# Kernel tuning notes

Hardware: AMD Instinct MI355X
Metric: run time of the kernel (lower is better)

## Reference

```python
import jax, jax.numpy as jnp
import numpy as np

N_STATE = 1024
N_HEAD = 16
HEAD_DIM = N_STATE // N_HEAD


def setup_inputs() -> dict:
    key = jax.random.key(0)
    ks = jax.random.split(key, 8)
    s = 0.02
    return {
        "x": jax.random.normal(ks[0], (4, 1500, N_STATE), dtype=jnp.float32),
        "Wq": jax.random.normal(ks[1], (N_STATE, N_STATE), dtype=jnp.float32) * s,
        "bq": jnp.zeros((N_STATE,), dtype=jnp.float32),
        "Wk": jax.random.normal(ks[2], (N_STATE, N_STATE), dtype=jnp.float32) * s,
        "Wv": jax.random.normal(ks[3], (N_STATE, N_STATE), dtype=jnp.float32) * s,
        "bv": jnp.zeros((N_STATE,), dtype=jnp.float32),
        "Wo": jax.random.normal(ks[4], (N_STATE, N_STATE), dtype=jnp.float32) * s,
        "bo": jnp.zeros((N_STATE,), dtype=jnp.float32),
    }


def reference(x, Wq, bq, Wk, Wv, bv, Wo, bo):
    B, S, _ = x.shape
    scale = HEAD_DIM ** (-0.5)
    # projections (torch Linear: y = x @ W.T + b)
    q = x @ Wq.T + bq
    k = x @ Wk.T
    v = x @ Wv.T + bv
    # [B, H, S, D]
    q = q.reshape(B, S, N_HEAD, HEAD_DIM).transpose(0, 2, 1, 3)
    k = k.reshape(B, S, N_HEAD, HEAD_DIM).transpose(0, 2, 1, 3)
    v = v.reshape(B, S, N_HEAD, HEAD_DIM).transpose(0, 2, 1, 3)
    # scores scaled AFTER the matmul, as in the original (qk * qk_scale)
    qk = jnp.einsum("bhqd,bhkd->bhqk", q, k) * scale
    w = jax.nn.softmax(qk, axis=-1)
    wv = jnp.einsum("bhqk,bhkd->bhqd", w, v)
    wv = wv.transpose(0, 2, 1, 3).reshape(B, S, N_STATE)
    return wv @ Wo.T + bo
```

## Files before the change

### kernel.cpp

```cpp
#include <hip/hip_runtime.h>
#include <stdint.h>

#define S_LEN  1500
#define S_PAD  1536
#define BATCH  4
#define NSTATE 1024
#define NHEAD  16
#define HDIM   64
#define MROWS  6000
#define C1 0.180336879f

typedef __attribute__((ext_vector_type(8)))  short short8;
typedef __attribute__((ext_vector_type(4)))  float floatx4;
typedef __attribute__((ext_vector_type(16))) float floatx16;

__device__ __forceinline__ unsigned short f2bf(float f) {
  union { float f; unsigned int u; } v; v.f = f;
  unsigned int r = v.u + 0x7fffu + ((v.u >> 16) & 1u);
  return (unsigned short)(r >> 16);
}

__device__ __forceinline__ void gld_lds16(const void* g, void* l) {
  __builtin_amdgcn_global_load_lds(
      (const __attribute__((address_space(1))) void*)g,
      (__attribute__((address_space(3))) void*)l, 16, 0, 0);
}

__global__ __launch_bounds__(256) void cvt_all(
    const float* __restrict__ x,  const float* __restrict__ Wq,
    const float* __restrict__ Wk, const float* __restrict__ Wv,
    const float* __restrict__ Wo, unsigned short* __restrict__ dst)
{
  const size_t NX = (size_t)MROWS * NSTATE;
  size_t e = ((size_t)blockIdx.x * 256 + threadIdx.x) * 4;
  const float* src; size_t off;
  if (e < NX) { src = x; off = e; }
  else {
    size_t t = e - NX;
    int wsel = (int)(t >> 20);
    off = t & ((1u << 20) - 1);
    src = (wsel == 0) ? Wq : (wsel == 1) ? Wk : (wsel == 2) ? Wv : Wo;
  }
  float4 v = *(const float4*)(src + off);
  uint2 o;
  o.x = (unsigned int)f2bf(v.x) | ((unsigned int)f2bf(v.y) << 16);
  o.y = (unsigned int)f2bf(v.z) | ((unsigned int)f2bf(v.w) << 16);
  *(uint2*)(dst + e) = o;
}

template <bool F32OUT>
__device__ __forceinline__ void gemm128_bt(
    const unsigned short* __restrict__ X,
    const unsigned short* __restrict__ W,
    const float* __restrict__ bias,
    void* __restrict__ Yv,
    int m0, int n0, float oscale)
{
  __shared__ unsigned short As[2][128 * 32];
  __shared__ unsigned short Bs[2][128 * 32];

  const int tid  = threadIdx.x;
  const int lane = tid & 63;
  const int wid  = tid >> 6;
  const int wm   = (wid & 1) * 64;
  const int wn   = (wid >> 1) * 64;
  const int l15  = lane & 15;
  const int l4   = lane >> 4;

  floatx4 acc[4][4];
#pragma unroll
  for (int i = 0; i < 4; ++i)
#pragma unroll
    for (int j = 0; j < 4; ++j)
      acc[i][j] = (floatx4){0.f, 0.f, 0.f, 0.f};

  const int srow  = tid >> 2;
  const int scolb = (tid & 3) * 16;

  const char* xrp[2];
  const char* wrp[2];
#pragma unroll
  for (int r = 0; r < 2; ++r) {
    int arow = m0 + r * 64 + srow;
    if (arow > MROWS - 1) arow = MROWS - 1;
    xrp[r] = (const char*)X + (size_t)arow * NSTATE * 2 + scolb;
    int brow = n0 + r * 64 + srow;
    wrp[r] = (const char*)W + (size_t)brow * NSTATE * 2 + scolb;
  }

  for (int k0 = 0; k0 < NSTATE; k0 += 64) {
    __syncthreads();
#pragma unroll
    for (int h = 0; h < 2; ++h) {
      int kb = (k0 + h * 32) * 2;
#pragma unroll
      for (int r = 0; r < 2; ++r) {
        gld_lds16(xrp[r] + kb, (char*)As[h] + r * 4096 + wid * 1024);
        gld_lds16(wrp[r] + kb, (char*)Bs[h] + r * 4096 + wid * 1024);
      }
    }
    __syncthreads();

#pragma unroll
    for (int h = 0; h < 2; ++h) {
      short8 a[4], b[4];
#pragma unroll
      for (int i = 0; i < 4; ++i)
        a[i] = *(const short8*)(As[h] + (wm + i * 16 + l15) * 32 + l4 * 8);
#pragma unroll
      for (int j = 0; j < 4; ++j)
        b[j] = *(const short8*)(Bs[h] + (wn + j * 16 + l15) * 32 + l4 * 8);
#pragma unroll
      for (int i = 0; i < 4; ++i)
#pragma unroll
        for (int j = 0; j < 4; ++j)
          acc[i][j] = __builtin_amdgcn_mfma_f32_16x16x32_bf16(a[i], b[j], acc[i][j], 0, 0, 0);
    }
  }

#pragma unroll
  for (int j = 0; j < 4; ++j) {
    int ng = n0 + wn + j * 16 + l15;
    float bias_v = bias ? bias[ng] : 0.f;
#pragma unroll
    for (int i = 0; i < 4; ++i) {
      int mgb = m0 + wm + i * 16 + l4 * 4;
#pragma unroll
      for (int r = 0; r < 4; ++r) {
        int mg = mgb + r;
        if (mg < MROWS) {
          float val = (acc[i][j][r] + bias_v) * oscale;
          if (F32OUT) ((float*)Yv)[(size_t)mg * NSTATE + ng] = val;
          else        ((unsigned short*)Yv)[(size_t)mg * NSTATE + ng] = f2bf(val);
        }
      }
    }
  }
}

__global__ __launch_bounds__(256) void proj_qkv(
    const unsigned short* __restrict__ X,
    const unsigned short* __restrict__ Wq, const unsigned short* __restrict__ Wk,
    const unsigned short* __restrict__ Wv,
    const float* __restrict__ bq, const float* __restrict__ bv,
    unsigned short* __restrict__ q, unsigned short* __restrict__ k,
    unsigned short* __restrict__ v)
{
  const int id  = blockIdx.x;
  const int sid = (id & 7) * 141 + (id >> 3);
  const int z   = sid / 376;
  const int rem = sid - z * 376;
  const int m0  = (rem >> 3) * 128;
  const int n0  = (rem & 7) * 128;

  const unsigned short* W = (z == 0) ? Wq : (z == 1) ? Wk : Wv;
  const float* bias       = (z == 0) ? bq : (z == 1) ? (const float*)nullptr : bv;
  unsigned short* Y       = (z == 0) ? q  : (z == 1) ? k  : v;
  const float osc         = (z == 0) ? C1 : 1.0f;
  gemm128_bt<false>(X, W, bias, Y, m0, n0, osc);
}

__global__ __launch_bounds__(256) void proj_o(
    const unsigned short* __restrict__ X, const unsigned short* __restrict__ W,
    const float* __restrict__ bias, float* __restrict__ Y)
{
  const int id  = blockIdx.x;
  const int sid = (id & 7) * 47 + (id >> 3);
  gemm128_bt<true>(X, W, bias, Y, (sid >> 3) * 128, (sid & 7) * 128, 1.0f);
}

__global__ __launch_bounds__(256) void vtrans(
    const unsigned short* __restrict__ v, unsigned short* __restrict__ vt)
{
  __shared__ unsigned short T[64][72];
  const int tid = threadIdx.x;
  const int st = blockIdx.x * 64, h = blockIdx.y, b = blockIdx.z;
#pragma unroll
  for (int rr = 0; rr < 2; ++rr) {
    int sl = rr * 32 + (tid >> 3);
    int dl = (tid & 7) * 8;
    int s  = st + sl;
    uint4 val = make_uint4(0u, 0u, 0u, 0u);
    if (s < S_LEN)
      val = *(const uint4*)&v[((size_t)b * S_LEN + s) * NSTATE + h * HDIM + dl];
    *(uint4*)&T[sl][dl] = val;
  }
  __syncthreads();
#pragma unroll
  for (int rr = 0; rr < 2; ++rr) {
    int dl = rr * 32 + (tid >> 3);
    int s0 = (tid & 7) * 8;
    unsigned short tmp[8];
#pragma unroll
    for (int j2 = 0; j2 < 8; ++j2) tmp[j2] = T[s0 + j2][dl];
    *(uint4*)&vt[(((size_t)b * NHEAD + h) * HDIM + dl) * S_PAD + st + s0] =
        *(const uint4*)tmp;
  }
}

__global__ __launch_bounds__(256, 4) void attn32t(
    const unsigned short* __restrict__ Q, const unsigned short* __restrict__ K,
    const unsigned short* __restrict__ VT, unsigned short* __restrict__ O)
{
  __shared__ unsigned short SMEM[16384];
  unsigned short* Ks  = SMEM;
  unsigned short* Vts = SMEM + 8192;
  unsigned short* Os  = SMEM;

  const int tid  = threadIdx.x;
  const int lane = tid & 63;
  const int w    = tid >> 6;
  const int l31  = lane & 31;
  const int lhi  = lane >> 5;

  const int id  = blockIdx.x;
  const int sid = (id & 7) * 96 + (id >> 3);
  const int qt  = sid % 12;
  const int hb  = sid / 12;
  const int h   = hb & 15;
  const int b   = hb >> 4;

  const size_t base  = ((size_t)b * S_LEN) * NSTATE + h * HDIM;
  const size_t vbase = (((size_t)b * NHEAD + h) * HDIM) * S_PAD;

  short8 qf[4];
  {
    int qrow = qt * 128 + w * 32 + l31;
    if (qrow > S_LEN - 1) qrow = S_LEN - 1;
    const unsigned short* qp = Q + base + (size_t)qrow * NSTATE;
#pragma unroll
    for (int c = 0; c < 4; ++c)
      qf[c] = *(const short8*)(qp + c * 16 + lhi * 8);
  }

  short8 ones8;
#pragma unroll
  for (int i = 0; i < 8; ++i) ones8[i] = (short)0x3F80;

  floatx16 oacc[2];
  oacc[0] = (floatx16)(0.f);
  oacc[1] = (floatx16)(0.f);
  floatx16 lacc = (floatx16)(0.f);

  for (int t = 0; t < 12; ++t) {
    __syncthreads();
#pragma unroll
    for (int qq = 0; qq < 4; ++qq) {
      int row  = (w * 4 + qq) * 8 + (lane >> 3);
      int logc = (lane & 7) ^ (row & 7);
      int s = t * 128 + row; if (s > S_LEN - 1) s = S_LEN - 1;
      gld_lds16(&K[base + (size_t)s * NSTATE + logc * 8],
                (char*)Ks + (w * 4 + qq) * 1024);
    }
#pragma unroll
    for (int qq = 0; qq < 4; ++qq) {
      int d    = (w * 4 + qq) * 4 + (lane >> 4);
      int logc = (lane & 15) ^ (d & 7);
      gld_lds16(&VT[vbase + (size_t)d * S_PAD + t * 128 + logc * 8],
                (char*)Vts + (w * 4 + qq) * 1024);
    }
    __syncthreads();

#pragma unroll
    for (int kvt = 0; kvt < 4; ++kvt) {
      floatx16 sacc = (floatx16)(0.f);
#pragma unroll
      for (int c = 0; c < 4; ++c) {
        int row  = kvt * 32 + l31;
        int phys = (c * 2 + lhi) ^ (row & 7);
        short8 ak = *(const short8*)(Ks + row * 64 + phys * 8);
        sacc = __builtin_amdgcn_mfma_f32_32x32x16_bf16(ak, qf[c], sacc, 0, 0, 0);
      }

      if (t == 11 && kvt >= 2) {
        if (kvt == 3) {
#pragma unroll
          for (int r = 0; r < 16; ++r) sacc[r] = -3.0e38f;
        } else {
#pragma unroll
          for (int r = 12; r < 16; ++r) sacc[r] = lhi ? -3.0e38f : sacc[r];
        }
      }

      unsigned int pk[8], ex[8];
#pragma unroll
      for (int i = 0; i < 8; ++i) {
        float plo = exp2f(sacc[2 * i]);
        float phi = exp2f(sacc[2 * i + 1]);
        unsigned int rr;
        asm("v_cvt_pk_bf16_f32 %0, %1, %2" : "=v"(rr) : "v"(plo), "v"(phi));
        pk[i] = rr;
      }
#pragma unroll
      for (int i = 0; i < 8; ++i)
        ex[i] = __shfl_xor((unsigned int)pk[i], 32, 64);

      int4 f0i, f1i;
      f0i.x = lhi ? ex[2] : pk[0];
      f0i.y = lhi ? ex[3] : pk[1];
      f0i.z = lhi ? pk[2] : ex[0];
      f0i.w = lhi ? pk[3] : ex[1];
      f1i.x = lhi ? ex[6] : pk[4];
      f1i.y = lhi ? ex[7] : pk[5];
      f1i.z = lhi ? pk[6] : ex[4];
      f1i.w = lhi ? pk[7] : ex[5];
      short8 f0 = *(short8*)&f0i;
      short8 f1 = *(short8*)&f1i;

      lacc = __builtin_amdgcn_mfma_f32_32x32x16_bf16(ones8, f0, lacc, 0, 0, 0);
      lacc = __builtin_amdgcn_mfma_f32_32x32x16_bf16(ones8, f1, lacc, 0, 0, 0);

#pragma unroll
      for (int dt = 0; dt < 2; ++dt) {
        int d = dt * 32 + l31;
        int p0 = ((kvt * 4 + 0) + lhi) ^ (d & 7);
        int p1 = ((kvt * 4 + 2) + lhi) ^ (d & 7);
        short8 av0 = *(const short8*)(Vts + d * 128 + p0 * 8);
        short8 av1 = *(const short8*)(Vts + d * 128 + p1 * 8);
        oacc[dt] = __builtin_amdgcn_mfma_f32_32x32x16_bf16(av0, f0, oacc[dt], 0, 0, 0);
        oacc[dt] = __builtin_amdgcn_mfma_f32_32x32x16_bf16(av1, f1, oacc[dt], 0, 0, 0);
      }
    }
  }

  float inv = 1.f / lacc[0];

  __syncthreads();
#pragma unroll
  for (int dt = 0; dt < 2; ++dt)
#pragma unroll
    for (int g = 0; g < 4; ++g) {
      int d0 = dt * 32 + g * 8 + lhi * 4;
      float v0 = oacc[dt][4 * g + 0] * inv;
      float v1 = oacc[dt][4 * g + 1] * inv;
      float v2 = oacc[dt][4 * g + 2] * inv;
      float v3 = oacc[dt][4 * g + 3] * inv;
      uint2 pk2;
      pk2.x = (unsigned int)f2bf(v0) | ((unsigned int)f2bf(v1) << 16);
      pk2.y = (unsigned int)f2bf(v2) | ((unsigned int)f2bf(v3) << 16);
      *(uint2*)&Os[(w * 32 + l31) * 72 + d0] = pk2;
    }
  __syncthreads();
#pragma unroll
  for (int pass = 0; pass < 4; ++pass) {
    int e = pass * 256 + tid;
    int row = e >> 3, ch = e & 7;
    int s = qt * 128 + row;
    if (s < S_LEN)
      *(uint4*)&O[base + (size_t)s * NSTATE + ch * 8] = *(const uint4*)&Os[row * 72 + ch * 8];
  }
}

extern "C" void kernel_launch(void* const* d_in, const int* in_sizes, int n_in,
                              void* d_out, int out_size, void* d_ws, size_t ws_size,
                              hipStream_t stream) {
  const float* x  = (const float*)d_in[0];
  const float* Wq = (const float*)d_in[1];
  const float* bq = (const float*)d_in[2];
  const float* Wk = (const float*)d_in[3];
  const float* Wv = (const float*)d_in[4];
  const float* bv = (const float*)d_in[5];
  const float* Wo = (const float*)d_in[6];
  const float* bo = (const float*)d_in[7];
  float* out = (float*)d_out;

  const size_t NX = (size_t)MROWS * NSTATE;
  const size_t NW = (size_t)NSTATE * NSTATE;

  unsigned short* xb  = (unsigned short*)d_ws;
  unsigned short* Wqb = xb  + NX;
  unsigned short* Wkb = Wqb + NW;
  unsigned short* Wvb = Wkb + NW;
  unsigned short* Wob = Wvb + NW;
  unsigned short* q   = Wob + NW;
  unsigned short* k   = q + NX;
  unsigned short* v   = k + NX;
  unsigned short* vt  = v + NX;
  unsigned short* wv  = xb;

  dim3 blk(256);
  const size_t n4_total = (NX + 4 * NW) / 4;
  cvt_all<<<dim3((int)(n4_total / 256)), blk, 0, stream>>>(x, Wq, Wk, Wv, Wo, xb);
  proj_qkv<<<dim3(1128), blk, 0, stream>>>(xb, Wqb, Wkb, Wvb, bq, bv, q, k, v);
  vtrans<<<dim3(24, NHEAD, BATCH), blk, 0, stream>>>(v, vt);
  attn32t<<<dim3(768), blk, 0, stream>>>(q, k, vt, wv);
  proj_o<<<dim3(376), blk, 0, stream>>>(wv, Wob, bo, out);
}
```

Before: 255.7 us.

## Double-buffer 64-key K/V tiles in attention loop with prefetch and MFMA priority

Splits each 128-key K/V tile into 64-key halves stored in two LDS buffers, so the loads for the next half are issued before the current half is computed. This leaves one barrier per step instead of two and overlaps the global-to-LDS copies with the MFMA work. It also raises wave priority around the MFMA sections via s_setprio. The LDS footprint stays at 32KB, but there are twice as many loop iterations. Because global_load_lds writes into the other buffer asynchronously, correctness depends on the barrier at the end of each step being enough for the vmcnt wait.

```diff
diff --git a/kernel.cpp b/kernel.cpp
--- a/kernel.cpp
+++ b/kernel.cpp
@@ -198,14 +198,14 @@
   }
 }
 
+#define NHALF 24
+
 __global__ __launch_bounds__(256, 4) void attn32t(
     const unsigned short* __restrict__ Q, const unsigned short* __restrict__ K,
     const unsigned short* __restrict__ VT, unsigned short* __restrict__ O)
 {
   __shared__ unsigned short SMEM[16384];
-  unsigned short* Ks  = SMEM;
-  unsigned short* Vts = SMEM + 8192;
-  unsigned short* Os  = SMEM;
+  unsigned short* Os = SMEM;
 
   const int tid  = threadIdx.x;
   const int lane = tid & 63;
@@ -223,6 +223,9 @@
   const size_t base  = ((size_t)b * S_LEN) * NSTATE + h * HDIM;
   const size_t vbase = (((size_t)b * NHEAD + h) * HDIM) * S_PAD;
 
+  const int srow8 = lane >> 3;
+  const int sc3   = lane & 7;
+
   short8 qf[4];
   {
     int qrow = qt * 128 + w * 32 + l31;
@@ -242,38 +245,52 @@
   oacc[1] = (floatx16)(0.f);
   floatx16 lacc = (floatx16)(0.f);
 
-  for (int t = 0; t < 12; ++t) {
-    __syncthreads();
-#pragma unroll
-    for (int qq = 0; qq < 4; ++qq) {
-      int row  = (w * 4 + qq) * 8 + (lane >> 3);
-      int logc = (lane & 7) ^ (row & 7);
-      int s = t * 128 + row; if (s > S_LEN - 1) s = S_LEN - 1;
-      gld_lds16(&K[base + (size_t)s * NSTATE + logc * 8],
-                (char*)Ks + (w * 4 + qq) * 1024);
-    }
-#pragma unroll
-    for (int qq = 0; qq < 4; ++qq) {
-      int d    = (w * 4 + qq) * 4 + (lane >> 4);
-      int logc = (lane & 15) ^ (d & 7);
-      gld_lds16(&VT[vbase + (size_t)d * S_PAD + t * 128 + logc * 8],
-                (char*)Vts + (w * 4 + qq) * 1024);
-    }
-    __syncthreads();
-
-#pragma unroll
-    for (int kvt = 0; kvt < 4; ++kvt) {
+  auto stage_half = [&](int u, int bi) {
+    char* kbase = (char*)SMEM + bi * 8192;
+    char* vbase_l = (char*)SMEM + 16384 + bi * 8192;
+#pragma unroll
+    for (int qq = 0; qq < 2; ++qq) {
+      int cg   = w * 2 + qq;
+      int row  = cg * 8 + srow8;
+      int logc = sc3 ^ (row & 7);
+      int s = u * 64 + row; if (s > S_LEN - 1) s = S_LEN - 1;
+      gld_lds16(&K[base + (size_t)s * NSTATE + logc * 8], kbase + cg * 1024);
+    }
+#pragma unroll
+    for (int qq = 0; qq < 2; ++qq) {
+      int cg   = w * 2 + qq;
+      int d    = cg * 8 + srow8;
+      int logc = sc3 ^ (d & 7);
+      gld_lds16(&VT[vbase + (size_t)d * S_PAD + u * 64 + logc * 8],
+                vbase_l + cg * 1024);
+    }
+  };
+
+  stage_half(0, 0);
+  __syncthreads();
+
+  for (int u = 0; u < NHALF; ++u) {
+    const int cur = u & 1;
+    if (u < NHALF - 1) stage_half(u + 1, cur ^ 1);
+
+    const unsigned short* Ks  = SMEM + cur * 4096;
+    const unsigned short* Vts = SMEM + 8192 + cur * 4096;
+
+#pragma unroll
+    for (int kvt = 0; kvt < 2; ++kvt) {
+      int row = kvt * 32 + l31;
       floatx16 sacc = (floatx16)(0.f);
+      __builtin_amdgcn_s_setprio(1);
 #pragma unroll
       for (int c = 0; c < 4; ++c) {
-        int row  = kvt * 32 + l31;
         int phys = (c * 2 + lhi) ^ (row & 7);
         short8 ak = *(const short8*)(Ks + row * 64 + phys * 8);
         sacc = __builtin_amdgcn_mfma_f32_32x32x16_bf16(ak, qf[c], sacc, 0, 0, 0);
       }
-
-      if (t == 11 && kvt >= 2) {
-        if (kvt == 3) {
+      __builtin_amdgcn_s_setprio(0);
+
+      if (u == NHALF - 1) {
+        if (kvt == 1) {
 #pragma unroll
           for (int r = 0; r < 16; ++r) sacc[r] = -3.0e38f;
         } else {
@@ -307,6 +324,7 @@
       short8 f0 = *(short8*)&f0i;
       short8 f1 = *(short8*)&f1i;
 
+      __builtin_amdgcn_s_setprio(1);
       lacc = __builtin_amdgcn_mfma_f32_32x32x16_bf16(ones8, f0, lacc, 0, 0, 0);
       lacc = __builtin_amdgcn_mfma_f32_32x32x16_bf16(ones8, f1, lacc, 0, 0, 0);
 
@@ -315,12 +333,15 @@
         int d = dt * 32 + l31;
         int p0 = ((kvt * 4 + 0) + lhi) ^ (d & 7);
         int p1 = ((kvt * 4 + 2) + lhi) ^ (d & 7);
-        short8 av0 = *(const short8*)(Vts + d * 128 + p0 * 8);
-        short8 av1 = *(const short8*)(Vts + d * 128 + p1 * 8);
+        short8 av0 = *(const short8*)(Vts + d * 64 + p0 * 8);
+        short8 av1 = *(const short8*)(Vts + d * 64 + p1 * 8);
         oacc[dt] = __builtin_amdgcn_mfma_f32_32x32x16_bf16(av0, f0, oacc[dt], 0, 0, 0);
         oacc[dt] = __builtin_amdgcn_mfma_f32_32x32x16_bf16(av1, f1, oacc[dt], 0, 0, 0);
       }
-    }
+      __builtin_amdgcn_s_setprio(0);
+    }
+
+    __syncthreads();
   }
 
   float inv = 1.f / lacc[0];
```

Result: no change. 255.9 us (+0.1%).
